# Kernel tuning notes

Hardware: AMD Instinct MI355X
Metric: run time of the kernel (lower is better)

The kernel has to match this reference:

```python
import jax, jax.numpy as jnp
import numpy as np

H, B, F, D1, D21, D22, C = 10, 16384, 4, 2048, 2048, 2048, 2
OBS_X, OBS_Y, RADIUS = 40.0, 15.0, 6.0


def setup_inputs() -> dict:
    key = jax.random.key(0)
    ks = jax.random.split(key, 12)
    s = 0.02  # weight scale
    return {
        'x':   jax.random.normal(ks[0], (B, F), jnp.float32),
        'W1':  jax.random.normal(ks[1], (H, F, D1), jnp.float32) * s,
        'b1':  jnp.zeros((H, D1), jnp.float32),
        'W21': jax.random.normal(ks[2], (H, D1, D21), jnp.float32) * s,
        'b21': jnp.zeros((H, D21), jnp.float32),
        'W22': jax.random.normal(ks[3], (H, D1, D22), jnp.float32) * s,
        'b22': jnp.zeros((H, D22), jnp.float32),
        'W31': jax.random.normal(ks[4], (H, D21, C), jnp.float32) * s,
        'b31': jnp.zeros((H, C), jnp.float32),
        'W32': jax.random.normal(ks[5], (H, D22, C), jnp.float32) * s,
        'b32': jnp.zeros((H, C), jnp.float32),
        'wt':  jnp.ones((H,), jnp.float32),
        'mean': jax.random.normal(ks[6], (F,), jnp.float32),
        'std':  jnp.ones((F,), jnp.float32),
        'sgn': 1,
        'itr': 0,
    }


def reference(x, W1, b1, W21, b21, W22, b22, W31, b31, W32, b32, wt, mean, std, sgn, itr):
    # x: [B,F]; un-normalized state x0 = x*std + mean
    x0 = x * std + mean

    # --- 10-head small-MLP ensemble (batched over heads via einsum) ---
    h1  = jax.nn.relu(jnp.einsum('bf,hfd->hbd', x, W1) + b1[:, None, :])      # [H,B,D1]
    x21 = jax.nn.relu(jnp.einsum('hbd,hde->hbe', h1, W21) + b21[:, None, :])  # [H,B,D21]
    x22 = jax.nn.relu(jnp.einsum('hbd,hde->hbe', h1, W22) + b22[:, None, :])  # [H,B,D22]
    x31 = jnp.einsum('hbe,hec->hbc', x21, W31) + b31[:, None, :]              # [H,B,C] nominal control
    x32 = 4.0 * jax.nn.sigmoid(jnp.einsum('hbe,hec->hbc', x22, W32) + b32[:, None, :])  # [H,B,C] CBF params

    # --- dCBF constraint (shared across heads; depends only on x0) ---
    px, py, theta, v = x0[:, 0], x0[:, 1], x0[:, 2], x0[:, 3]
    dx, dy = px - OBS_X, py - OBS_Y
    st, ct = jnp.sin(theta), jnp.cos(theta)
    barrier = dx * dx + dy * dy - RADIUS * RADIUS                 # [B]
    barrier_dot = 2.0 * dx * v * ct + 2.0 * dy * v * st          # [B]
    Lf2b = 2.0 * v * v                                            # [B]
    LgLfbu1 = -2.0 * dx * v * st + 2.0 * dy * v * ct
    LgLfbu2 = 2.0 * dx * ct + 2.0 * dy * st
    G = jnp.stack([-LgLfbu1, -LgLfbu2], axis=-1)                  # [B,C]

    # sgn == 1 -> same branch for every head (i==0 or sgn==1)
    h_rhs = Lf2b + (x32[..., 0] + x32[..., 1]) * barrier_dot + x32[..., 0] * x32[..., 1] * barrier  # [H,B]

    # --- batched QP: min 0.5 u'u - x31'u  s.t. G u <= h  (Q = I) ---
    # closed-form single-constraint active set: u = x31 - relu(G.x31 - h)/||G||^2 * G
    Gu = jnp.einsum('bc,hbc->hb', G, x31)                         # [H,B]
    GG = jnp.sum(G * G, axis=-1)                                  # [B]
    lam = jax.nn.relu(Gu - h_rhs) / GG                            # [H,B]
    u = x31 - lam[..., None] * G[None, :, :]                      # [H,B,C]

    # --- softmax-weighted ensemble sum ---
    w = jax.nn.softmax(wt)                                        # [H]
    return jnp.einsum('h,hbc->bc', w, u)                          # [B,C]
```

## Files before the change

kernel.cpp:

```cpp
#include <hip/hip_runtime.h>
#include <hip/hip_bf16.h>
#include <stdint.h>

#define H_  10
#define B_  16384
#define F_  4
#define D_  2048
#define C_  2

typedef __attribute__((ext_vector_type(8))) short  short8;
typedef __attribute__((ext_vector_type(4))) float  floatx4;

typedef const uint32_t __attribute__((address_space(1))) gu32;
typedef uint32_t       __attribute__((address_space(3))) lu32;

__device__ __forceinline__ void async16(const void* g, void* l) {
    __builtin_amdgcn_global_load_lds((gu32*)g, (lu32*)l, 16, 0, 0);
}

__device__ __forceinline__ short8 bc8(uint4 v) { return __builtin_bit_cast(short8, v); }

__device__ __forceinline__ uint32_t packbf(float a, float b) {
    a = fmaxf(a, 0.f); b = fmaxf(b, 0.f);
    const uint32_t ax = __builtin_bit_cast(uint32_t, a) + 0x8000u;
    const uint32_t bx = __builtin_bit_cast(uint32_t, b) + 0x8000u;
    return (ax >> 16) | (bx & 0xFFFF0000u);
}

__device__ __forceinline__ uint32_t f2bf(float f) {
    union { float f; uint32_t u; } a; a.f = f;
    uint32_t u = a.u;
    u += 0x7FFF + ((u >> 16) & 1);
    return u >> 16;
}
__device__ __forceinline__ uint32_t pack2bf(float a, float b) {
    return f2bf(a) | (f2bf(b) << 16);
}


__global__ __launch_bounds__(256) void k_convert(
    const float* __restrict__ W21, const float* __restrict__ W22,
    uint16_t* __restrict__ Bc)
{
    __shared__ float tile[64][65];
    const int z = blockIdx.z;
    const int h = z % H_;
    const float* src = (z < H_ ? W21 : W22) + (size_t)h * D_ * D_;
    uint16_t*   dst  = Bc + (size_t)h * 2 * D_ * D_ + (z < H_ ? 0 : (size_t)D_ * D_);
    const int k0 = blockIdx.x * 64, n0 = blockIdx.y * 64;
    const int t = threadIdx.x;

    const int c4 = (t & 15) * 4;
    const int rb = (t >> 4) * 4;
#pragma unroll
    for (int i = 0; i < 4; i++) {
        const float4 v = *(const float4*)(src + (size_t)(k0 + rb + i) * D_ + n0 + c4);
        tile[rb + i][c4 + 0] = v.x; tile[rb + i][c4 + 1] = v.y;
        tile[rb + i][c4 + 2] = v.z; tile[rb + i][c4 + 3] = v.w;
    }
    __syncthreads();
    const int n = t >> 2;
    const int cb = (t & 3) * 2;
#pragma unroll
    for (int j = 0; j < 2; j++) {
        const int kk = (cb + j) * 8;
        uint32_t pk[4];
#pragma unroll
        for (int e = 0; e < 4; e++)
            pk[e] = pack2bf(tile[kk + 2 * e][n], tile[kk + 2 * e + 1][n]);
        *(uint4*)(dst + (size_t)(n0 + n) * D_ + k0 + kk) = make_uint4(pk[0], pk[1], pk[2], pk[3]);
    }
}

__global__ __launch_bounds__(256) void k_zero(uint4* p, int n4) {
    const int i = blockIdx.x * 256 + threadIdx.x;
    if (i < n4) p[i] = make_uint4(0u, 0u, 0u, 0u);
}

__global__ __launch_bounds__(256) void k_h1(
    const float* __restrict__ x, const float* __restrict__ W1,
    const float* __restrict__ b1, uint16_t* __restrict__ h1t, int h)
{
    const int t = threadIdx.x;
    const int kc = t & 127;
    const int rh = t >> 7;
    const int k0 = kc * 16;
    const float* W1h = W1 + (size_t)h * F_ * D_;
    float w[4][16], bb[16];
#pragma unroll
    for (int f = 0; f < 4; f++)
#pragma unroll
        for (int j = 0; j < 16; j += 4) {
            const float4 v = *(const float4*)(W1h + f * D_ + k0 + j);
            w[f][j] = v.x; w[f][j+1] = v.y; w[f][j+2] = v.z; w[f][j+3] = v.w;
        }
#pragma unroll
    for (int j = 0; j < 16; j += 4) {
        const float4 v = *(const float4*)(b1 + (size_t)h * D_ + k0 + j);
        bb[j] = v.x; bb[j+1] = v.y; bb[j+2] = v.z; bb[j+3] = v.w;
    }
    const int rowBase = blockIdx.x * 16 + rh * 8;
#pragma unroll
    for (int rr = 0; rr < 8; rr++) {
        const int row = rowBase + rr;
        const float4 xv = *(const float4*)(x + (size_t)row * 4);
        uint32_t pk[8];
#pragma unroll
        for (int j = 0; j < 16; j += 2) {
            float aa = fmaf(xv.x, w[0][j], bb[j]);
            aa = fmaf(xv.y, w[1][j], aa);
            aa = fmaf(xv.z, w[2][j], aa);
            aa = fmaf(xv.w, w[3][j], aa);
            float bv = fmaf(xv.x, w[0][j+1], bb[j+1]);
            bv = fmaf(xv.y, w[1][j+1], bv);
            bv = fmaf(xv.z, w[2][j+1], bv);
            bv = fmaf(xv.w, w[3][j+1], bv);
            pk[j >> 1] = packbf(aa, bv);
        }
        uint16_t* d = h1t + (size_t)row * D_ + k0;
        *(uint4*)d       = make_uint4(pk[0], pk[1], pk[2], pk[3]);
        *(uint4*)(d + 8) = make_uint4(pk[4], pk[5], pk[6], pk[7]);
    }
}

__global__ __launch_bounds__(512, 2) void k_gemm(
    const uint16_t* __restrict__ h1t, const uint16_t* __restrict__ Bc,
    const float* __restrict__ b21, const float* __restrict__ b22,
    const float* __restrict__ W31, const float* __restrict__ W32,
    float* __restrict__ acc31, float* __restrict__ acc32, int h)
{
    extern __shared__ uint4 smem[];
    uint4* Asl = smem;
    uint4* Bsl = smem + 4096;

    const int bid = blockIdx.x;
    const int wg  = (bid & 7) * 128 + (bid >> 3);
    const int mBase = (wg & 63) * 256;
    const int nBase = (wg >> 6) * 256;

    const int t = threadIdx.x;
    const int lane = t & 63, wid = t >> 6;
    const int c15 = lane & 15, q = lane >> 4;
    const int wm = wid >> 2, wn = wid & 3;

    const int srow   = lane >> 3;
    const int schunk = (lane & 7) ^ srow;
    const int sldA   = wid * 64;

    const uint16_t* Ag = h1t + (size_t)(mBase + wid * 8 + srow) * D_ + schunk * 8;
    const uint16_t* Bg = Bc + (size_t)h * (4096 * (size_t)D_)
                            + (size_t)(nBase + wid * 8 + srow) * D_ + schunk * 8;

    auto stageA = [&](int buf, int half, int kt) {
#pragma unroll
        for (int i = 0; i < 2; i++)
            async16(Ag + (size_t)((half * 128 + i * 64) * D_ + kt),
                    Asl + buf * 2048 + half * 1024 + i * 512 + sldA);
    };
    auto stageB = [&](int buf, int half, int kt) {
#pragma unroll
        for (int i = 0; i < 2; i++)
            async16(Bg + (size_t)((half * 128 + i * 64) * D_ + kt),
                    Bsl + buf * 2048 + half * 1024 + i * 512 + sldA);
    };

    const int axor  = c15 & 7;
    const int ck0   = q ^ axor;
    const int ck1   = (q + 4) ^ axor;
    const int abase = (wm * 128 + c15) * 8;
    const int bbase = (wn * 64 + c15) * 8;

    floatx4 acc[8][4];
    const floatx4 z4 = {0.f, 0.f, 0.f, 0.f};
#pragma unroll
    for (int mi = 0; mi < 8; mi++)
#pragma unroll
        for (int ni = 0; ni < 4; ni++) acc[mi][ni] = z4;

    stageA(0, 0, 0);  stageA(0, 1, 0);
    stageB(0, 0, 0);  stageB(0, 1, 0);
    stageA(1, 0, 64); stageA(1, 1, 64);
    asm volatile("s_waitcnt vmcnt(4)" ::: "memory");
    __builtin_amdgcn_sched_barrier(0);
    __builtin_amdgcn_s_barrier();

    int cur = 0;
    for (int tt = 0; tt < 32; ++tt) {
        const int ktB = (tt < 31 ? tt + 1 : 31) * 64;
        const int ktA = (tt < 30 ? tt + 2 : 31) * 64;
        const uint4* Ab = Asl + cur * 2048;
        const uint4* Bb = Bsl + cur * 2048;
        const int nxt = cur ^ 1;

        short8 a0[4][2], a1[4][2], b0f[2][2], b1f[2][2];

#pragma unroll
        for (int mi = 0; mi < 4; mi++) {
            a0[mi][0] = bc8(Ab[abase + mi * 128 + ck0]);
            a0[mi][1] = bc8(Ab[abase + mi * 128 + ck1]);
        }
#pragma unroll
        for (int ni = 0; ni < 2; ni++) {
            b0f[ni][0] = bc8(Bb[bbase + ni * 128 + ck0]);
            b0f[ni][1] = bc8(Bb[bbase + ni * 128 + ck1]);
        }
        __builtin_amdgcn_s_barrier();
        asm volatile("s_waitcnt lgkmcnt(0)" ::: "memory");
        __builtin_amdgcn_sched_barrier(0);
        __builtin_amdgcn_s_setprio(1);
#pragma unroll
        for (int mi = 0; mi < 4; mi++)
#pragma unroll
            for (int ni = 0; ni < 2; ni++) {
                acc[mi][ni] = __builtin_amdgcn_mfma_f32_16x16x32_bf16(a0[mi][0], b0f[ni][0], acc[mi][ni], 0, 0, 0);
                acc[mi][ni] = __builtin_amdgcn_mfma_f32_16x16x32_bf16(a0[mi][1], b0f[ni][1], acc[mi][ni], 0, 0, 0);
            }
        __builtin_amdgcn_s_setprio(0);
        __builtin_amdgcn_s_barrier();

#pragma unroll
        for (int ni = 0; ni < 2; ni++) {
            b1f[ni][0] = bc8(Bb[bbase + (ni + 2) * 128 + ck0]);
            b1f[ni][1] = bc8(Bb[bbase + (ni + 2) * 128 + ck1]);
        }
        stageB(nxt, 0, ktB);
        __builtin_amdgcn_s_barrier();
        asm volatile("s_waitcnt lgkmcnt(0)" ::: "memory");
        __builtin_amdgcn_sched_barrier(0);
        __builtin_amdgcn_s_setprio(1);
#pragma unroll
        for (int mi = 0; mi < 4; mi++)
#pragma unroll
            for (int ni = 0; ni < 2; ni++) {
                acc[mi][ni + 2] = __builtin_amdgcn_mfma_f32_16x16x32_bf16(a0[mi][0], b1f[ni][0], acc[mi][ni + 2], 0, 0, 0);
                acc[mi][ni + 2] = __builtin_amdgcn_mfma_f32_16x16x32_bf16(a0[mi][1], b1f[ni][1], acc[mi][ni + 2], 0, 0, 0);
            }
        __builtin_amdgcn_s_setprio(0);
        __builtin_amdgcn_s_barrier();

#pragma unroll
        for (int mi = 0; mi < 4; mi++) {
            a1[mi][0] = bc8(Ab[abase + (mi + 4) * 128 + ck0]);
            a1[mi][1] = bc8(Ab[abase + (mi + 4) * 128 + ck1]);
        }
        stageB(nxt, 1, ktB);
        __builtin_amdgcn_s_barrier();
        asm volatile("s_waitcnt lgkmcnt(0)" ::: "memory");
        __builtin_amdgcn_sched_barrier(0);
        __builtin_amdgcn_s_setprio(1);
#pragma unroll
        for (int mi = 0; mi < 4; mi++)
#pragma unroll
            for (int ni = 0; ni < 2; ni++) {
                acc[mi + 4][ni] = __builtin_amdgcn_mfma_f32_16x16x32_bf16(a1[mi][0], b0f[ni][0], acc[mi + 4][ni], 0, 0, 0);
                acc[mi + 4][ni] = __builtin_amdgcn_mfma_f32_16x16x32_bf16(a1[mi][1], b0f[ni][1], acc[mi + 4][ni], 0, 0, 0);
            }
        __builtin_amdgcn_s_setprio(0);
        __builtin_amdgcn_s_barrier();

        stageA(cur, 0, ktA);
        stageA(cur, 1, ktA);
        asm volatile("s_waitcnt vmcnt(4)" ::: "memory");
        __builtin_amdgcn_sched_barrier(0);
        __builtin_amdgcn_s_barrier();
        __builtin_amdgcn_s_setprio(1);
#pragma unroll
        for (int mi = 0; mi < 4; mi++)
#pragma unroll
            for (int ni = 0; ni < 2; ni++) {
                acc[mi + 4][ni + 2] = __builtin_amdgcn_mfma_f32_16x16x32_bf16(a1[mi][0], b1f[ni][0], acc[mi + 4][ni + 2], 0, 0, 0);
                acc[mi + 4][ni + 2] = __builtin_amdgcn_mfma_f32_16x16x32_bf16(a1[mi][1], b1f[ni][1], acc[mi + 4][ni + 2], 0, 0, 0);
            }
        __builtin_amdgcn_s_setprio(0);
        __builtin_amdgcn_s_barrier();

        cur = nxt;
    }

    const int p    = nBase >> 11;
    const int nloc = nBase & 2047;
    const float* b2p = (p ? b22 : b21) + (size_t)h * D_;
    const float* W3p = (p ? W32 : W31) + (size_t)h * D_ * C_;
    float* ab = (p ? acc32 : acc31) + (size_t)h * B_ * C_;

    float w3x[4], w3y[4], bs[4];
#pragma unroll
    for (int ni = 0; ni < 4; ni++) {
        const int e = nloc + wn * 64 + ni * 16 + c15;
        bs[ni] = b2p[e];
        const float2 w2 = *(const float2*)(W3p + e * 2);
        w3x[ni] = w2.x; w3y[ni] = w2.y;
    }
#pragma unroll
    for (int mi = 0; mi < 8; mi++) {
        float s0[4], s1[4];
#pragma unroll
        for (int r = 0; r < 4; r++) {
            float t0 = 0.f, t1 = 0.f;
#pragma unroll
            for (int ni = 0; ni < 4; ni++) {
                float v = fmaxf(acc[mi][ni][r] + bs[ni], 0.f);
                t0 = fmaf(v, w3x[ni], t0);
                t1 = fmaf(v, w3y[ni], t1);
            }
            s0[r] = t0; s1[r] = t1;
        }
#pragma unroll
        for (int off = 1; off < 16; off <<= 1)
#pragma unroll
            for (int r = 0; r < 4; r++) {
                s0[r] += __shfl_xor(s0[r], off, 64);
                s1[r] += __shfl_xor(s1[r], off, 64);
            }
        if (c15 == 0) {
#pragma unroll
            for (int r = 0; r < 4; r++) {
                const int row = mBase + wm * 128 + mi * 16 + q * 4 + r;
                atomicAdd(&ab[row * C_ + 0], s0[r]);
                atomicAdd(&ab[row * C_ + 1], s1[r]);
            }
        }
    }
}

__global__ __launch_bounds__(256) void k_final(
    const float* __restrict__ x,
    const float* __restrict__ acc31, const float* __restrict__ acc32,
    const float* __restrict__ b31, const float* __restrict__ b32,
    const float* __restrict__ wt, const float* __restrict__ mean,
    const float* __restrict__ stdv, float* __restrict__ out)
{
    const int b = blockIdx.x * 256 + threadIdx.x;
    const float4 xb = *(const float4*)(x + (size_t)b * 4);
    const float px = xb.x * stdv[0] + mean[0];
    const float py = xb.y * stdv[1] + mean[1];
    const float th = xb.z * stdv[2] + mean[2];
    const float v  = xb.w * stdv[3] + mean[3];
    const float dx = px - 40.0f, dy = py - 15.0f;
    const float st = sinf(th), ct = cosf(th);
    const float barrier = dx * dx + dy * dy - 36.0f;
    const float bdot = 2.f * dx * v * ct + 2.f * dy * v * st;
    const float Lf2b = 2.f * v * v;
    const float G0 = -(-2.f * dx * v * st + 2.f * dy * v * ct);
    const float G1 = -(2.f * dx * ct + 2.f * dy * st);
    const float GG = G0 * G0 + G1 * G1;

    float we[H_];
    float wmax = wt[0];
    for (int h = 1; h < H_; h++) wmax = fmaxf(wmax, wt[h]);
    float wsum = 0.f;
    for (int h = 0; h < H_; h++) { we[h] = expf(wt[h] - wmax); wsum += we[h]; }

    float o0 = 0.f, o1 = 0.f;
#pragma unroll
    for (int h = 0; h < H_; h++) {
        const size_t idx = ((size_t)h * B_ + b) * 2;
        const float x310 = acc31[idx]     + b31[h * 2];
        const float x311 = acc31[idx + 1] + b31[h * 2 + 1];
        const float z0 = acc32[idx]     + b32[h * 2];
        const float z1 = acc32[idx + 1] + b32[h * 2 + 1];
        const float x320 = 4.f / (1.f + expf(-z0));
        const float x321 = 4.f / (1.f + expf(-z1));
        const float hr = Lf2b + (x320 + x321) * bdot + x320 * x321 * barrier;
        const float Gu = G0 * x310 + G1 * x311;
        const float lam = fmaxf(Gu - hr, 0.f) / GG;
        o0 += we[h] * (x310 - lam * G0);
        o1 += we[h] * (x311 - lam * G1);
    }
    out[b * 2]     = o0 / wsum;
    out[b * 2 + 1] = o1 / wsum;
}

extern "C" void kernel_launch(void* const* d_in, const int* in_sizes, int n_in,
                              void* d_out, int out_size, void* d_ws, size_t ws_size,
                              hipStream_t stream)
{
    const float* x    = (const float*)d_in[0];
    const float* W1   = (const float*)d_in[1];
    const float* b1   = (const float*)d_in[2];
    const float* W21  = (const float*)d_in[3];
    const float* b21  = (const float*)d_in[4];
    const float* W22  = (const float*)d_in[5];
    const float* b22  = (const float*)d_in[6];
    const float* W31  = (const float*)d_in[7];
    const float* b31  = (const float*)d_in[8];
    const float* W32  = (const float*)d_in[9];
    const float* b32  = (const float*)d_in[10];
    const float* wt   = (const float*)d_in[11];
    const float* mean = (const float*)d_in[12];
    const float* stdv = (const float*)d_in[13];
    float* out = (float*)d_out;

    char* ws = (char*)d_ws;
    uint16_t* Bc   = (uint16_t*)(ws);
    float* acc31   = (float*)(ws + 167772160);
    float* acc32   = (float*)(ws + 169082880);
    uint16_t* h1t  = (uint16_t*)(ws + 170393600);

    static bool attr_done = false;
    if (!attr_done) {
        hipFuncSetAttribute(reinterpret_cast<const void*>(k_gemm),
                            hipFuncAttributeMaxDynamicSharedMemorySize, 131072);
        attr_done = true;
    }

    k_convert<<<dim3(32, 32, 20), 256, 0, stream>>>(W21, W22, Bc);
    k_zero<<<dim3(640), 256, 0, stream>>>((uint4*)acc31, 163840);
    for (int h = 0; h < H_; ++h) {
        k_h1<<<dim3(1024), 256, 0, stream>>>(x, W1, b1, h1t, h);
        k_gemm<<<dim3(1024), 512, 131072, stream>>>(h1t, Bc, b21, b22, W31, W32,
                                                    acc31, acc32, h);
    }
    k_final<<<dim3(64), 256, 0, stream>>>(x, acc31, acc32, b31, b32, wt, mean, stdv, out);
}
```

Before: 3.828 ms.

## Restructure GEMM main loop to prefetch next-tile fragments and use partial LDS waits

Rewrites the k_gemm inner loop so each stage's full A and B tiles are staged with four async loads per call. The MFMA quadrants are reordered so the next k-tile's a0/b0 register fragments are read from LDS at the end of the current iteration. Full lgkmcnt(0) waits become partial counts, and barriers per iteration drop from eight to four, so LDS reads can overlap MFMA issue. The tighter counting creates a risk of LDS read/write races when a buffer is refilled while earlier fragment reads may still be in flight.

```diff
diff --git a/kernel.cpp b/kernel.cpp
--- a/kernel.cpp
+++ b/kernel.cpp
@@ -124,7 +124,7 @@
 }
 
 __global__ __launch_bounds__(512, 2) void k_gemm(
-    const uint16_t* __restrict__ h1t, const uint16_t* __restrict__ Bc,
+    const uint16_t* __restrict__ h1t, const uint16_t* __restrict__ Bcw,
     const float* __restrict__ b21, const float* __restrict__ b22,
     const float* __restrict__ W31, const float* __restrict__ W32,
     float* __restrict__ acc31, float* __restrict__ acc32, int h)
@@ -148,20 +148,20 @@
     const int sldA   = wid * 64;
 
     const uint16_t* Ag = h1t + (size_t)(mBase + wid * 8 + srow) * D_ + schunk * 8;
-    const uint16_t* Bg = Bc + (size_t)h * (4096 * (size_t)D_)
-                            + (size_t)(nBase + wid * 8 + srow) * D_ + schunk * 8;
-
-    auto stageA = [&](int buf, int half, int kt) {
-#pragma unroll
-        for (int i = 0; i < 2; i++)
-            async16(Ag + (size_t)((half * 128 + i * 64) * D_ + kt),
-                    Asl + buf * 2048 + half * 1024 + i * 512 + sldA);
+    const uint16_t* Bg = Bcw + (size_t)h * (4096 * (size_t)D_)
+                             + (size_t)(nBase + wid * 8 + srow) * D_ + schunk * 8;
+
+    auto stageA = [&](int buf, int kt) {
+#pragma unroll
+        for (int i = 0; i < 4; i++)
+            async16(Ag + (size_t)(i * 64) * D_ + kt,
+                    Asl + buf * 2048 + i * 512 + sldA);
     };
-    auto stageB = [&](int buf, int half, int kt) {
-#pragma unroll
-        for (int i = 0; i < 2; i++)
-            async16(Bg + (size_t)((half * 128 + i * 64) * D_ + kt),
-                    Bsl + buf * 2048 + half * 1024 + i * 512 + sldA);
+    auto stageB = [&](int buf, int kt) {
+#pragma unroll
+        for (int i = 0; i < 4; i++)
+            async16(Bg + (size_t)(i * 64) * D_ + kt,
+                    Bsl + buf * 2048 + i * 512 + sldA);
     };
 
     const int axor  = c15 & 7;
@@ -177,104 +177,107 @@
 #pragma unroll
         for (int ni = 0; ni < 4; ni++) acc[mi][ni] = z4;
 
-    stageA(0, 0, 0);  stageA(0, 1, 0);
-    stageB(0, 0, 0);  stageB(0, 1, 0);
-    stageA(1, 0, 64); stageA(1, 1, 64);
-    asm volatile("s_waitcnt vmcnt(4)" ::: "memory");
+    short8 a0[4][2], a1[4][2], b0[2][2], b1[2][2];
+
+    stageA(0, 0);   stageB(0, 0);
+    stageA(1, 64);  stageB(1, 64);
+    asm volatile("s_waitcnt vmcnt(8)" ::: "memory");
     __builtin_amdgcn_sched_barrier(0);
     __builtin_amdgcn_s_barrier();
-
-    int cur = 0;
+#pragma unroll
+    for (int mi = 0; mi < 4; mi++) {
+        a0[mi][0] = bc8(Asl[abase + mi * 128 + ck0]);
+        a0[mi][1] = bc8(Asl[abase + mi * 128 + ck1]);
+    }
+#pragma unroll
+    for (int ni = 0; ni < 2; ni++) {
+        b0[ni][0] = bc8(Bsl[bbase + ni * 128 + ck0]);
+        b0[ni][1] = bc8(Bsl[bbase + ni * 128 + ck1]);
+    }
+
     for (int tt = 0; tt < 32; ++tt) {
-        const int ktB = (tt < 31 ? tt + 1 : 31) * 64;
-        const int ktA = (tt < 30 ? tt + 2 : 31) * 64;
-        const uint4* Ab = Asl + cur * 2048;
+        const int cur = tt & 1, nxt = cur ^ 1;
+        const uint4* Ac = Asl + cur * 2048;
         const uint4* Bb = Bsl + cur * 2048;
-        const int nxt = cur ^ 1;
-
-        short8 a0[4][2], a1[4][2], b0f[2][2], b1f[2][2];
+        const uint4* An = Asl + nxt * 2048;
+        const uint4* Bn = Bsl + nxt * 2048;
+        const int kt2 = (tt < 30 ? tt + 2 : 31) * 64;
 
 #pragma unroll
         for (int mi = 0; mi < 4; mi++) {
-            a0[mi][0] = bc8(Ab[abase + mi * 128 + ck0]);
-            a0[mi][1] = bc8(Ab[abase + mi * 128 + ck1]);
-        }
-#pragma unroll
-        for (int ni = 0; ni < 2; ni++) {
-            b0f[ni][0] = bc8(Bb[bbase + ni * 128 + ck0]);
-            b0f[ni][1] = bc8(Bb[bbase + ni * 128 + ck1]);
-        }
-        __builtin_amdgcn_s_barrier();
-        asm volatile("s_waitcnt lgkmcnt(0)" ::: "memory");
+            a1[mi][0] = bc8(Ac[abase + (mi + 4) * 128 + ck0]);
+            a1[mi][1] = bc8(Ac[abase + (mi + 4) * 128 + ck1]);
+        }
+        asm volatile("s_waitcnt lgkmcnt(8)" ::: "memory");
         __builtin_amdgcn_sched_barrier(0);
         __builtin_amdgcn_s_setprio(1);
 #pragma unroll
         for (int mi = 0; mi < 4; mi++)
 #pragma unroll
             for (int ni = 0; ni < 2; ni++) {
-                acc[mi][ni] = __builtin_amdgcn_mfma_f32_16x16x32_bf16(a0[mi][0], b0f[ni][0], acc[mi][ni], 0, 0, 0);
-                acc[mi][ni] = __builtin_amdgcn_mfma_f32_16x16x32_bf16(a0[mi][1], b0f[ni][1], acc[mi][ni], 0, 0, 0);
+                acc[mi][ni] = __builtin_amdgcn_mfma_f32_16x16x32_bf16(a0[mi][0], b0[ni][0], acc[mi][ni], 0, 0, 0);
+                acc[mi][ni] = __builtin_amdgcn_mfma_f32_16x16x32_bf16(a0[mi][1], b0[ni][1], acc[mi][ni], 0, 0, 0);
             }
         __builtin_amdgcn_s_setprio(0);
         __builtin_amdgcn_s_barrier();
 
+        stageA(cur, kt2);
 #pragma unroll
         for (int ni = 0; ni < 2; ni++) {
-            b1f[ni][0] = bc8(Bb[bbase + (ni + 2) * 128 + ck0]);
-            b1f[ni][1] = bc8(Bb[bbase + (ni + 2) * 128 + ck1]);
-        }
-        stageB(nxt, 0, ktB);
-        __builtin_amdgcn_s_barrier();
-        asm volatile("s_waitcnt lgkmcnt(0)" ::: "memory");
+            b1[ni][0] = bc8(Bb[bbase + (ni + 2) * 128 + ck0]);
+            b1[ni][1] = bc8(Bb[bbase + (ni + 2) * 128 + ck1]);
+        }
+        asm volatile("s_waitcnt lgkmcnt(4)" ::: "memory");
         __builtin_amdgcn_sched_barrier(0);
         __builtin_amdgcn_s_setprio(1);
 #pragma unroll
         for (int mi = 0; mi < 4; mi++)
 #pragma unroll
             for (int ni = 0; ni < 2; ni++) {
-                acc[mi][ni + 2] = __builtin_amdgcn_mfma_f32_16x16x32_bf16(a0[mi][0], b1f[ni][0], acc[mi][ni + 2], 0, 0, 0);
-                acc[mi][ni + 2] = __builtin_amdgcn_mfma_f32_16x16x32_bf16(a0[mi][1], b1f[ni][1], acc[mi][ni + 2], 0, 0, 0);
+                acc[mi + 4][ni] = __builtin_amdgcn_mfma_f32_16x16x32_bf16(a1[mi][0], b0[ni][0], acc[mi + 4][ni], 0, 0, 0);
+                acc[mi + 4][ni] = __builtin_amdgcn_mfma_f32_16x16x32_bf16(a1[mi][1], b0[ni][1], acc[mi + 4][ni], 0, 0, 0);
             }
         __builtin_amdgcn_s_setprio(0);
-        __builtin_amdgcn_s_barrier();
-
-#pragma unroll
-        for (int mi = 0; mi < 4; mi++) {
-            a1[mi][0] = bc8(Ab[abase + (mi + 4) * 128 + ck0]);
-            a1[mi][1] = bc8(Ab[abase + (mi + 4) * 128 + ck1]);
-        }
-        stageB(nxt, 1, ktB);
-        __builtin_amdgcn_s_barrier();
-        asm volatile("s_waitcnt lgkmcnt(0)" ::: "memory");
-        __builtin_amdgcn_sched_barrier(0);
-        __builtin_amdgcn_s_setprio(1);
-#pragma unroll
-        for (int mi = 0; mi < 4; mi++)
-#pragma unroll
-            for (int ni = 0; ni < 2; ni++) {
-                acc[mi + 4][ni] = __builtin_amdgcn_mfma_f32_16x16x32_bf16(a1[mi][0], b0f[ni][0], acc[mi + 4][ni], 0, 0, 0);
-                acc[mi + 4][ni] = __builtin_amdgcn_mfma_f32_16x16x32_bf16(a1[mi][1], b0f[ni][1], acc[mi + 4][ni], 0, 0, 0);
-            }
-        __builtin_amdgcn_s_setprio(0);
-        __builtin_amdgcn_s_barrier();
-
-        stageA(cur, 0, ktA);
-        stageA(cur, 1, ktA);
         asm volatile("s_waitcnt vmcnt(4)" ::: "memory");
         __builtin_amdgcn_sched_barrier(0);
         __builtin_amdgcn_s_barrier();
+
+        stageB(cur, kt2);
+#pragma unroll
+        for (int ni = 0; ni < 2; ni++) {
+            b0[ni][0] = bc8(Bn[bbase + ni * 128 + ck0]);
+            b0[ni][1] = bc8(Bn[bbase + ni * 128 + ck1]);
+        }
+        asm volatile("s_waitcnt lgkmcnt(4)" ::: "memory");
+        __builtin_amdgcn_sched_barrier(0);
         __builtin_amdgcn_s_setprio(1);
 #pragma unroll
         for (int mi = 0; mi < 4; mi++)
 #pragma unroll
             for (int ni = 0; ni < 2; ni++) {
-                acc[mi + 4][ni + 2] = __builtin_amdgcn_mfma_f32_16x16x32_bf16(a1[mi][0], b1f[ni][0], acc[mi + 4][ni + 2], 0, 0, 0);
-                acc[mi + 4][ni + 2] = __builtin_amdgcn_mfma_f32_16x16x32_bf16(a1[mi][1], b1f[ni][1], acc[mi + 4][ni + 2], 0, 0, 0);
+                acc[mi][ni + 2] = __builtin_amdgcn_mfma_f32_16x16x32_bf16(a0[mi][0], b1[ni][0], acc[mi][ni + 2], 0, 0, 0);
+                acc[mi][ni + 2] = __builtin_amdgcn_mfma_f32_16x16x32_bf16(a0[mi][1], b1[ni][1], acc[mi][ni + 2], 0, 0, 0);
             }
         __builtin_amdgcn_s_setprio(0);
         __builtin_amdgcn_s_barrier();
 
-        cur = nxt;
+#pragma unroll
+        for (int mi = 0; mi < 4; mi++) {
+            a0[mi][0] = bc8(An[abase + mi * 128 + ck0]);
+            a0[mi][1] = bc8(An[abase + mi * 128 + ck1]);
+        }
+        asm volatile("s_waitcnt lgkmcnt(12)" ::: "memory");
+        __builtin_amdgcn_sched_barrier(0);
+        __builtin_amdgcn_s_setprio(1);
+#pragma unroll
+        for (int mi = 0; mi < 4; mi++)
+#pragma unroll
+            for (int ni = 0; ni < 2; ni++) {
+                acc[mi + 4][ni + 2] = __builtin_amdgcn_mfma_f32_16x16x32_bf16(a1[mi][0], b1[ni][0], acc[mi + 4][ni + 2], 0, 0, 0);
+                acc[mi + 4][ni + 2] = __builtin_amdgcn_mfma_f32_16x16x32_bf16(a1[mi][1], b1[ni][1], acc[mi + 4][ni + 2], 0, 0, 0);
+            }
+        __builtin_amdgcn_s_setprio(0);
+        __builtin_amdgcn_s_barrier();
     }
 
     const int p    = nBase >> 11;
```

New measurement: 4.432 ms. +15.8%, slower.
